# Optimization experiments

Measured on AMD Instinct MI355X. Metric: run time of the kernel, lower is better.

## Reference

```python
import jax, jax.numpy as jnp
from jax import lax
import numpy as np

SQRT2 = 1.4142135623730951
STYLE_DIM = 512
MOD_SCALE = 1.0 / np.sqrt(float(STYLE_DIM))          # EqualLinear modulation, lr_mul=1
MAP_SCALE = 0.01 / np.sqrt(float(STYLE_DIM))          # mapping EqualLinear, lr_mul=0.01
LR_MUL = 0.01


def _blur_kernel():
    k = np.array([1.0, 3.0, 3.0, 1.0], dtype=np.float32)
    k = k[None, :] * k[:, None]
    return jnp.asarray(k / k.sum())


def upfirdn2d(x, k, up=1, down=1, pad=(0, 0)):
    # torch upfirdn2d inserts (up-1) zeros AFTER each sample -> extra trailing pad of up-1
    C = x.shape[1]
    kern = jnp.tile(k[None, None], (C, 1, 1, 1))  # depthwise [C,1,kh,kw] (kernel symmetric, no flip needed)
    p = (pad[0], pad[1] + up - 1)
    return lax.conv_general_dilated(x, kern, (down, down), [p, p], lhs_dilation=(up, up),
                                    dimension_numbers=('NCHW', 'OIHW', 'NCHW'), feature_group_count=C)


def fused_lrelu(x, b):
    return jax.nn.leaky_relu(x + b.reshape(1, -1, 1, 1), 0.2) * SQRT2


def grouped_conv(x, w, pad, up):
    # x: [B,I,H,W], w: [B,O,I,k,k] per-sample weights -> grouped conv with B groups
    B, O, I, kh, kw = w.shape
    xg = x.reshape(1, B * I, x.shape[2], x.shape[3])
    if up:
        # torch conv_transpose2d(stride=2, padding=0) == dilated conv with spatially flipped kernel
        wf = jnp.flip(w, (-2, -1)).reshape(B * O, I, kh, kw)
        out = lax.conv_general_dilated(xg, wf, (1, 1), [(kh - 1, kh - 1), (kw - 1, kw - 1)],
                                       lhs_dilation=(2, 2),
                                       dimension_numbers=('NCHW', 'OIHW', 'NCHW'), feature_group_count=B)
    else:
        out = lax.conv_general_dilated(xg, w.reshape(B * O, I, kh, kw), (1, 1), [(pad, pad), (pad, pad)],
                                       dimension_numbers=('NCHW', 'OIHW', 'NCHW'), feature_group_count=B)
    return out.reshape(B, O, out.shape[2], out.shape[3])


def mod_conv(x, weight, style, mod_w, mod_b, demodulate, up, blur_k):
    # weight: [O,I,k,k]; style: [B,512]
    s = style @ (mod_w * MOD_SCALE).T + mod_b                       # [B,I]
    scale = 1.0 / np.sqrt(float(weight.shape[1] * weight.shape[2] * weight.shape[3]))
    w = scale * weight[None] * s[:, None, :, None, None]            # [B,O,I,k,k]
    if demodulate:
        d = lax.rsqrt(jnp.sum(w * w, axis=(2, 3, 4)) + 1e-8)
        w = w * d[:, :, None, None, None]
    out = grouped_conv(x, w, weight.shape[-1] // 2, up)
    if up:
        out = upfirdn2d(out, blur_k * 4.0, pad=(1, 1))              # Blur pad from p=len(k)-2-(3-1)=0
    return out


def _forward(z, mlp_w, mlp_b, const_input, conv_w, conv_mod_w, conv_mod_b, conv_bias,
             noise_strength, rgb_w, rgb_mod_w, rgb_mod_b, rgb_bias):
    B = z.shape[0]
    blur_k = _blur_kernel()
    w_lat = z * lax.rsqrt(jnp.mean(z * z, axis=1, keepdims=True) + 1e-8)
    for i in range(mlp_w.shape[0]):
        w_lat = jax.nn.leaky_relu(w_lat @ (mlp_w[i] * MAP_SCALE).T + mlp_b[i] * LR_MUL, 0.2) * SQRT2
    nkey = jax.random.key(7)

    def noise(l, shape):
        return jax.random.normal(jax.random.fold_in(nkey, l), (shape[0], 1, shape[2], shape[3]), dtype=jnp.float32)

    def styled(x, l, up):
        y = mod_conv(x, conv_w[l], w_lat, conv_mod_w[l], conv_mod_b[l], True, up, blur_k)
        y = y + noise_strength[l] * noise(l, y.shape)
        return fused_lrelu(y, conv_bias[l])

    def to_rgb(x, i):
        y = mod_conv(x, rgb_w[i], w_lat, rgb_mod_w[i], rgb_mod_b[i], False, False, blur_k)
        return y + rgb_bias[i].reshape(1, -1, 1, 1)

    out = jnp.tile(const_input, (B, 1, 1, 1))   # ConstantInput (shift=0 -> identity rolls)
    out = styled(out, 0, False)
    skip = to_rgb(out, 0)
    l = 1
    for blk in range(3):  # resolutions 8, 16, 32
        out = styled(out, l, True); l += 1
        out = styled(out, l, False); l += 1
        # Upsample(skip): kernel*factor^2, pad=(2,1), up=2
        skip = to_rgb(out, blk + 1) + upfirdn2d(skip, blur_k * 4.0, up=2, pad=(2, 1))
    return skip  # [B,3,32,32]


def setup_inputs() -> dict:
    key = jax.random.key(0)
    ks = jax.random.split(key, 8)
    B, S, C = 8, 512, 512
    return {
        'z': jax.random.normal(ks[0], (B, S), jnp.float32),
        'mlp_w': jax.random.normal(ks[1], (8, S, S), jnp.float32),
        'mlp_b': jnp.zeros((8, S), jnp.float32),
        'const_input': jax.random.normal(ks[2], (1, C, 4, 4), jnp.float32),
        'conv_w': jax.random.normal(ks[3], (7, C, C, 3, 3), jnp.float32),
        'conv_mod_w': jax.random.normal(ks[4], (7, C, S), jnp.float32),
        'conv_mod_b': jnp.ones((7, C), jnp.float32),
        'conv_bias': jnp.zeros((7, C), jnp.float32),
        'noise_strength': jax.random.normal(ks[5], (7,), jnp.float32) * 0.1,
        'rgb_w': jax.random.normal(ks[6], (4, 3, C, 1, 1), jnp.float32),
        'rgb_mod_w': jax.random.normal(ks[7], (4, C, S), jnp.float32),
        'rgb_mod_b': jnp.ones((4, C), jnp.float32),
        'rgb_bias': jnp.zeros((4, 3), jnp.float32),
    }


def reference(z, mlp_w, mlp_b, const_input, conv_w, conv_mod_w, conv_mod_b, conv_bias,
              noise_strength, rgb_w, rgb_mod_w, rgb_mod_b, rgb_bias):
    return _forward(z, mlp_w, mlp_b, const_input, conv_w, conv_mod_w, conv_mod_b, conv_bias,
                    noise_strength, rgb_w, rgb_mod_w, rgb_mod_b, rgb_bias)
```

## Files before the change

### kernel.cpp

```cpp
#include <hip/hip_runtime.h>


#define SQRT2F      1.41421356f
#define MAP_SCALE   4.41941738e-04f
#define MOD_SCALE   4.41941738e-02f
#define CONV_SCALE  1.47313913e-02f
#define RGB_SCALE   4.41941738e-02f

typedef __attribute__((ext_vector_type(8))) short bf16x8;
typedef __attribute__((ext_vector_type(16))) float f32x16;

__device__ __forceinline__ float bf2f(ushort u) {
    return __uint_as_float(((unsigned)u) << 16);
}
__device__ __forceinline__ ushort f2bf(float f) {
    unsigned u = __float_as_uint(f);
    unsigned r = (u + 0x7FFFu + ((u >> 16) & 1u)) >> 16;
    return (ushort)r;
}
__device__ __forceinline__ void store4bf(ushort* p, float a, float b, float c, float d) {
    union { ushort u[4]; uint2 v; } x;
    x.u[0] = f2bf(a); x.u[1] = f2bf(b); x.u[2] = f2bf(c); x.u[3] = f2bf(d);
    *(uint2*)p = x.v;
}

typedef __attribute__((address_space(1))) const unsigned int GAS;
typedef __attribute__((address_space(3))) unsigned int LAS;
__device__ __forceinline__ void gload_lds16(const ushort* g, ushort* l) {
    __builtin_amdgcn_global_load_lds((GAS*)g, (LAS*)l, 16, 0, 0);
}


__device__ __forceinline__ unsigned rotl32(unsigned x, int r) {
    return (x << r) | (x >> (32 - r));
}

__device__ void threefry2x32(unsigned k0, unsigned k1, unsigned x0, unsigned x1,
                             unsigned& o0, unsigned& o1) {
    unsigned k2 = k0 ^ k1 ^ 0x1BD11BDAu;
    x0 += k0; x1 += k1;
    x0 += x1; x1 = rotl32(x1,13); x1 ^= x0;
    x0 += x1; x1 = rotl32(x1,15); x1 ^= x0;
    x0 += x1; x1 = rotl32(x1,26); x1 ^= x0;
    x0 += x1; x1 = rotl32(x1, 6); x1 ^= x0;
    x0 += k1; x1 += k2 + 1u;
    x0 += x1; x1 = rotl32(x1,17); x1 ^= x0;
    x0 += x1; x1 = rotl32(x1,29); x1 ^= x0;
    x0 += x1; x1 = rotl32(x1,16); x1 ^= x0;
    x0 += x1; x1 = rotl32(x1,24); x1 ^= x0;
    x0 += k2; x1 += k0 + 2u;
    x0 += x1; x1 = rotl32(x1,13); x1 ^= x0;
    x0 += x1; x1 = rotl32(x1,15); x1 ^= x0;
    x0 += x1; x1 = rotl32(x1,26); x1 ^= x0;
    x0 += x1; x1 = rotl32(x1, 6); x1 ^= x0;
    x0 += k0; x1 += k1 + 3u;
    x0 += x1; x1 = rotl32(x1,17); x1 ^= x0;
    x0 += x1; x1 = rotl32(x1,29); x1 ^= x0;
    x0 += x1; x1 = rotl32(x1,16); x1 ^= x0;
    x0 += x1; x1 = rotl32(x1,24); x1 ^= x0;
    x0 += k1; x1 += k2 + 4u;
    x0 += x1; x1 = rotl32(x1,13); x1 ^= x0;
    x0 += x1; x1 = rotl32(x1,15); x1 ^= x0;
    x0 += x1; x1 = rotl32(x1,26); x1 ^= x0;
    x0 += x1; x1 = rotl32(x1, 6); x1 ^= x0;
    x0 += k2; x1 += k0 + 5u;
    o0 = x0; o1 = x1;
}

__device__ float bits_to_normal(unsigned bits) {
    unsigned m = (bits >> 9) | 0x3F800000u;
    float f = __uint_as_float(m) - 1.0f;
    const float lo = -0.99999994f;
    float u = f * 2.0f + lo;
    u = fmaxf(lo, u);
    float w = -log1pf(-u * u);
    float p;
    if (w < 5.0f) {
        w -= 2.5f;
        p = 2.81022636e-08f;
        p = fmaf(p, w, 3.43273939e-07f);
        p = fmaf(p, w, -3.5233877e-06f);
        p = fmaf(p, w, -4.39150654e-06f);
        p = fmaf(p, w, 0.00021858087f);
        p = fmaf(p, w, -0.00125372503f);
        p = fmaf(p, w, -0.00417768164f);
        p = fmaf(p, w, 0.246640727f);
        p = fmaf(p, w, 1.50140941f);
    } else {
        w = sqrtf(w) - 3.0f;
        p = -0.000200214257f;
        p = fmaf(p, w, 0.000100950558f);
        p = fmaf(p, w, 0.00134934322f);
        p = fmaf(p, w, -0.00367342844f);
        p = fmaf(p, w, 0.00573950773f);
        p = fmaf(p, w, -0.0076224613f);
        p = fmaf(p, w, 0.00943887047f);
        p = fmaf(p, w, 1.00167406f);
        p = fmaf(p, w, 2.83297682f);
    }
    return 1.41421354f * (p * u);
}

__global__ void noise_kernel(float* __restrict__ nbuf) {
    int g = blockIdx.x * 256 + threadIdx.x;
    if (g >= 21632) return;
    const int off[8] = {0, 128, 640, 1152, 3200, 5248, 13440, 21632};
    int l = 0;
    while (l < 6 && g >= off[l + 1]) l++;
    int i = g - off[l];
    unsigned k0, k1;
    threefry2x32(0u, 7u, 0u, (unsigned)l, k0, k1);
    unsigned b0, b1;
    threefry2x32(k0, k1, 0u, (unsigned)i, b0, b1);
    nbuf[g] = bits_to_normal(b0 ^ b1);
}


__global__ void pixelnorm_kernel(const float* __restrict__ z, float* __restrict__ out) {
    int b = blockIdx.x;
    int lane = threadIdx.x;
    float v[8];
    float s = 0.f;
    #pragma unroll
    for (int j = 0; j < 8; j++) {
        v[j] = z[b * 512 + lane + (j << 6)];
        s += v[j] * v[j];
    }
    #pragma unroll
    for (int off = 32; off > 0; off >>= 1) s += __shfl_xor(s, off, 64);
    float norm = rsqrtf(s * (1.f / 512.f) + 1e-8f);
    #pragma unroll
    for (int j = 0; j < 8; j++)
        out[b * 512 + lane + (j << 6)] = v[j] * norm;
}

__global__ void dot512_kernel(const float* __restrict__ win, const float* __restrict__ W,
                              const float* __restrict__ bias, float* __restrict__ out,
                              int total, float wscale, float bscale, int mode) {
    int gt = blockIdx.x * blockDim.x + threadIdx.x;
    int wv = gt >> 6;
    int lane = gt & 63;
    if (wv >= total) return;
    int l = wv >> 12;
    int r = wv & 4095;
    int b = r >> 9;
    int o = r & 511;
    const float* wrow = W + ((size_t)(l * 512 + o) << 9);
    const float* xrow = win + ((size_t)b << 9);
    float s = 0.f;
    #pragma unroll
    for (int j = 0; j < 8; j++) {
        int k = lane + (j << 6);
        s += wrow[k] * xrow[k];
    }
    #pragma unroll
    for (int off = 32; off > 0; off >>= 1) s += __shfl_xor(s, off, 64);
    if (lane == 0) {
        float v = s * wscale + bias[l * 512 + o] * bscale;
        if (mode) v = (v > 0.f ? v : 0.2f * v) * SQRT2F;
        out[wv] = v;
    }
}

__global__ __launch_bounds__(256) void wbconv_all(const float* __restrict__ cw,
                                                  ushort* __restrict__ wb7,
                                                  float* __restrict__ wsq7) {
    __shared__ float lg[288 * 65];
    const int bid = blockIdx.x;
    const int l = bid >> 7, rem = bid & 127, c = rem >> 3, og = rem & 7;
    const int o0 = og * 64;
    const int ibase = c * 32;
    const int tid = threadIdx.x;
    const int flip = (l == 1 || l == 3 || l == 5);

    #pragma unroll
    for (int r = 0; r < 18; r++) {
        int u = tid + 256 * r;
        int o = u / 72, w = u % 72;
        const float* src = cw + ((size_t)((l * 512 + o0 + o) * 512 + ibase)) * 9 + w * 4;
        float4 v = *(const float4*)src;
        lg[(w * 4 + 0) * 65 + o] = v.x;
        lg[(w * 4 + 1) * 65 + o] = v.y;
        lg[(w * 4 + 2) * 65 + o] = v.z;
        lg[(w * 4 + 3) * 65 + o] = v.w;
    }
    __syncthreads();

    #pragma unroll
    for (int r = 0; r < 8; r++) {
        int u = tid + 256 * r;
        int o = u >> 5, il = u & 31;
        float s = 0.f;
        #pragma unroll
        for (int t = 0; t < 9; t++) {
            float x = lg[(il * 9 + t) * 65 + o];
            s += x * x;
        }
        wsq7[((size_t)(l * 512 + o0 + o)) * 512 + ibase + il] = s;
    }

    ushort* wb = wb7 + (size_t)l * 2359296;
    #pragma unroll
    for (int r = 0; r < 9; r++) {
        int u = tid + 256 * r;
        int o = u & 63, tk = u >> 6;
        int t = tk >> 2, kv = tk & 3;
        int tsrc = flip ? (8 - t) : t;
        union { ushort us[8]; uint4 v; } pk;
        #pragma unroll
        for (int e = 0; e < 8; e++)
            pk.us[e] = f2bf(lg[((kv * 8 + e) * 9 + tsrc) * 65 + o]);
        *(uint4*)&wb[(size_t)(((c * 9 + t) * 4 + kv) * 512 + o0 + o) * 8] = pk.v;
    }
}

__global__ void demod_all(const float* __restrict__ wsq7, const float* __restrict__ sc,
                          float* __restrict__ dm) {
    int gt = blockIdx.x * blockDim.x + threadIdx.x;
    int wv = gt >> 6;
    int lane = gt & 63;
    if (wv >= 7 * 4096) return;
    int l = wv >> 12, b = (wv >> 9) & 7, o = wv & 511;
    const float* wr = wsq7 + (size_t)l * 262144 + ((size_t)o << 9);
    const float* sr = sc + l * 4096 + (b << 9);
    float s = 0.f;
    #pragma unroll
    for (int j = 0; j < 8; j++) {
        int k = lane + (j << 6);
        float sv = sr[k];
        s += wr[k] * sv * sv;
    }
    #pragma unroll
    for (int off = 32; off > 0; off >>= 1) s += __shfl_xor(s, off, 64);
    if (lane == 0) dm[wv] = rsqrtf(s * (1.f / 4608.f) + 1e-8f);
}

__global__ void prep0_kernel(const float* __restrict__ cinp, const float* __restrict__ s0,
                             ushort* __restrict__ X0p) {
    int gid = blockIdx.x * 256 + threadIdx.x;
    if (gid >= 8 * 36 * 64) return;
    int grp = gid & 63;
    int r = gid >> 6;
    int b = r / 36, rc = r % 36, row = rc / 6, col = rc % 6;
    int y = row - 1, x = col - 1;
    union { ushort u[8]; bf16x8 v; } pk;
    if (y >= 0 && y < 4 && x >= 0 && x < 4) {
        #pragma unroll
        for (int k = 0; k < 8; k++) {
            int ch = grp * 8 + k;
            pk.u[k] = f2bf(cinp[ch * 16 + y * 4 + x] * s0[b * 512 + ch]);
        }
    } else {
        #pragma unroll
        for (int k = 0; k < 8; k++) pk.u[k] = 0;
    }
    *(bf16x8*)&X0p[((size_t)grp * 288 + r) * 8] = pk.v;
}

template <int S, int NTILE, int WROWS, int KS, bool WUP>
__global__ __launch_bounds__(512, 1) void conv_dense6(
    const ushort* __restrict__ Xp, const ushort* __restrict__ wb,
    const float* __restrict__ dm, const float* __restrict__ nz,
    const float* __restrict__ nstr, const float* __restrict__ bias,
    const float* __restrict__ snext,
    ushort* __restrict__ T, ushort* __restrict__ XU, float* __restrict__ Pp) {
    constexpr int SP = S + 2, P2 = S * S, N = 8 * P2;
    constexpr int PXT = 8 * SP * SP;
    constexpr int JCOLS = NTILE / 128;
    constexpr int NPX = WROWS * SP;
    constexpr int ASZ = 9 * 4 * 64 * 8;
    constexpr int BSZ = NPX * 32;
    constexpr int PAIR = ASZ + BSZ;
    constexpr int NAU = 2304;
    constexpr int NAT = 5;
    constexpr int NBU = NPX * 4;
    constexpr int NBT = (NBU + 511) / 512;
    constexpr int ROWMAX = 8 * SP - 1;
    constexpr int CK = 16 / KS;
    constexpr int DB = (CK > 1) ? 2 : 1;
    constexpr int NAF = 4;
    constexpr int NBF = NBU / 512;
    constexpr int NMIN = NAF + NBF;
    constexpr int REDU = JCOLS * 16384;
    constexpr int LDSZ = (DB * PAIR > REDU) ? DB * PAIR : REDU;
    __shared__ __align__(16) ushort lds[LDSZ];

    const int tid = threadIdx.x, lane = tid & 63, nw = tid >> 6;
    const int sw = nw >> 2, nww = nw & 3;
    const int hf = lane >> 5, l31 = lane & 31;
    const int o0 = blockIdx.x * 64;
    const int n0 = blockIdx.y * NTILE;
    const int ks = blockIdx.z;
    const int R0 = (n0 / P2) * SP + (n0 % P2) / S;
    const int kvw = sw * 2 + hf;

    int pixbase[JCOLS], nj[JCOLS];
    #pragma unroll
    for (int j = 0; j < JCOLS; j++) {
        int n = n0 + nww * (NTILE / 4) + j * 32 + l31;
        nj[j] = n;
        int b = n / P2, r = n % P2;
        int y = r / S, x = r % S;
        pixbase[j] = (b * SP + y - R0) * SP + x;
    }
    f32x16 acc[JCOLS][2];
    #pragma unroll
    for (int j = 0; j < JCOLS; j++) { acc[j][0] = (f32x16)0.f; acc[j][1] = (f32x16)0.f; }

    int bgo[NBT];
    bool bgv[NBT];
    #pragma unroll
    for (int r = 0; r < NBT; r++) {
        int t = tid + 512 * r;
        bgv[r] = t < NBU;
        int tt = bgv[r] ? t : 0;
        int px = tt % NPX, kv = tt / NPX;
        int rr = px / SP, cc = px % SP;
        int Rc = R0 + rr; if (Rc > ROWMAX) Rc = ROWMAX;
        bgo[r] = (kv * PXT + Rc * SP + cc) * 8;
    }

    auto stage = [&](int cgi, int buf) {
        ushort* base = &lds[buf * PAIR];
        const ushort* asrc = wb + (size_t)cgi * 147456;
        #pragma unroll
        for (int r = 0; r < NAT; r++) {
            int u = tid + 512 * r;
            if (u < NAU) {
                int row = u >> 6;
                gload_lds16(asrc + ((size_t)(row * 512 + o0) + (u & 63)) * 8,
                            base + (r * 512 + nw * 64) * 8);
            }
        }
        const ushort* bsrc = Xp + (size_t)cgi * (PXT * 32);
        #pragma unroll
        for (int r = 0; r < NBT; r++)
            if (bgv[r])
                gload_lds16(bsrc + bgo[r], base + ASZ + (r * 512 + nw * 64) * 8);
    };

    stage(ks * CK, 0);
    for (int c = 0; c < CK; c++) {
        const int cur = c & 1;
        if (c + 1 < CK) {
            stage(ks * CK + c + 1, cur ^ 1);
            asm volatile("s_waitcnt vmcnt(%0)" :: "i"(NMIN) : "memory");
        } else {
            asm volatile("s_waitcnt vmcnt(0)" ::: "memory");
        }
        __builtin_amdgcn_s_barrier();
        __builtin_amdgcn_sched_barrier(0);
        const int bo = cur * PAIR;
        #pragma unroll
        for (int t = 0; t < 9; t++) {
            const int dpx = (t / 3) * SP + (t % 3);
            bf16x8 a0 = *(const bf16x8*)&lds[bo + ((t * 4 + kvw) * 64 + l31) * 8];
            bf16x8 a1 = *(const bf16x8*)&lds[bo + ((t * 4 + kvw) * 64 + 32 + l31) * 8];
            #pragma unroll
            for (int j = 0; j < JCOLS; j++) {
                bf16x8 bf = *(const bf16x8*)&lds[bo + ASZ + (kvw * NPX + pixbase[j] + dpx) * 8];
                acc[j][0] = __builtin_amdgcn_mfma_f32_32x32x16_bf16(a0, bf, acc[j][0], 0, 0, 0);
                acc[j][1] = __builtin_amdgcn_mfma_f32_32x32x16_bf16(a1, bf, acc[j][1], 0, 0, 0);
            }
        }
        __builtin_amdgcn_sched_barrier(0);
        __builtin_amdgcn_s_barrier();
    }

    #pragma unroll
    for (int j = 0; j < JCOLS; j++)
        #pragma unroll
        for (int sub = 0; sub < 2; sub++)
            #pragma unroll
            for (int rq = 0; rq < 4; rq++)
                if (sw == 1) {
                    int sidx = (j * 2 + sub) * 4 + rq;
                    float4 v = make_float4(acc[j][sub][rq * 4 + 0], acc[j][sub][rq * 4 + 1],
                                           acc[j][sub][rq * 4 + 2], acc[j][sub][rq * 4 + 3]);
                    *(float4*)&lds[sidx * 2048 + (nww * 64 + lane) * 8] = v;
                }
    __syncthreads();
    if (sw == 1) return;
    #pragma unroll
    for (int j = 0; j < JCOLS; j++)
        #pragma unroll
        for (int sub = 0; sub < 2; sub++)
            #pragma unroll
            for (int rq = 0; rq < 4; rq++) {
                int sidx = (j * 2 + sub) * 4 + rq;
                float4 p = *(const float4*)&lds[sidx * 2048 + (nww * 64 + lane) * 8];
                acc[j][sub][rq * 4 + 0] += p.x;
                acc[j][sub][rq * 4 + 1] += p.y;
                acc[j][sub][rq * 4 + 2] += p.z;
                acc[j][sub][rq * 4 + 3] += p.w;
            }

    if constexpr (KS > 1) {
        #pragma unroll
        for (int j = 0; j < JCOLS; j++) {
            float* pb = Pp + (((size_t)(ks * N + nj[j])) << 9) + o0;
            #pragma unroll
            for (int sub = 0; sub < 2; sub++) {
                #pragma unroll
                for (int rq = 0; rq < 4; rq++) {
                    float4 v = make_float4(acc[j][sub][rq * 4 + 0], acc[j][sub][rq * 4 + 1],
                                           acc[j][sub][rq * 4 + 2], acc[j][sub][rq * 4 + 3]);
                    *(float4*)&pb[sub * 32 + 4 * hf + 8 * rq] = v;
                }
            }
        }
        return;
    }
    float ns = nstr[0];
    #pragma unroll
    for (int j = 0; j < JCOLS; j++) {
        int n = nj[j], b = n / P2, r = n % P2;
        float nv = nz[b * P2 + r];
        int y = r / S, x = r % S;
        size_t tbase = (size_t)n << 9;
        int gpx = (b * SP + y + 1) * SP + x + 1;
        #pragma unroll
        for (int sub = 0; sub < 2; sub++) {
            #pragma unroll
            for (int rq = 0; rq < 4; rq++) {
                int o = o0 + sub * 32 + 4 * hf + 8 * rq;
                float4 d4 = *(const float4*)&dm[b * 512 + o];
                float4 b4 = *(const float4*)&bias[o];
                float vv[4];
                #pragma unroll
                for (int ri = 0; ri < 4; ri++) {
                    float v = acc[j][sub][rq * 4 + ri] * (&d4.x)[ri] * CONV_SCALE
                              + ns * nv + (&b4.x)[ri];
                    vv[ri] = (v > 0.f ? v : 0.2f * v) * SQRT2F;
                }
                store4bf(T + tbase + o, vv[0], vv[1], vv[2], vv[3]);
                if (WUP) {
                    float4 s4 = *(const float4*)&snext[b * 512 + o];
                    store4bf(XU + ((size_t)(o >> 3) * PXT + gpx) * 8 + (o & 7),
                             vv[0] * s4.x, vv[1] * s4.y, vv[2] * s4.z, vv[3] * s4.w);
                }
            }
        }
    }
}

template <int S, int KS, bool WUP>
__global__ void combine_dense(const float* __restrict__ Pp, const float* __restrict__ dm,
                              const float* __restrict__ nz, const float* __restrict__ nstr,
                              const float* __restrict__ bias, const float* __restrict__ snext,
                              ushort* __restrict__ T, ushort* __restrict__ XU) {
    constexpr int P2 = S * S, N = 8 * P2, SP = S + 2;
    constexpr int PXT = 8 * SP * SP;
    int gid = blockIdx.x * 256 + threadIdx.x;
    int n = gid >> 7, og = (gid & 127) << 2;
    float4 sm = make_float4(0.f, 0.f, 0.f, 0.f);
    #pragma unroll
    for (int k = 0; k < KS; k++) {
        float4 p = *(const float4*)&Pp[(((size_t)(k * N + n)) << 9) + og];
        sm.x += p.x; sm.y += p.y; sm.z += p.z; sm.w += p.w;
    }
    int b = n / P2, r = n % P2;
    float nsv = nstr[0] * nz[b * P2 + r];
    float4 d4 = *(const float4*)&dm[b * 512 + og];
    float4 b4 = *(const float4*)&bias[og];
    float vv[4];
    const float* sp = &sm.x;
    #pragma unroll
    for (int i = 0; i < 4; i++) {
        float v = sp[i] * (&d4.x)[i] * CONV_SCALE + nsv + (&b4.x)[i];
        vv[i] = (v > 0.f ? v : 0.2f * v) * SQRT2F;
    }
    store4bf(&T[((size_t)n << 9) + og], vv[0], vv[1], vv[2], vv[3]);
    if (WUP) {
        int y = r / S, x = r % S;
        int gpx = (b * SP + y + 1) * SP + x + 1;
        float4 s4 = *(const float4*)&snext[b * 512 + og];
        store4bf(&XU[((size_t)(og >> 3) * PXT + gpx) * 8 + (og & 7)],
                 vv[0] * s4.x, vv[1] * s4.y, vv[2] * s4.z, vv[3] * s4.w);
    }
}

template <int HIN, int NTILE, int WRW>
__global__ __launch_bounds__(256, 2) void conv_up5(
    const ushort* __restrict__ Xp, const ushort* __restrict__ wb,
    const float* __restrict__ dm, ushort* __restrict__ U) {
    constexpr int SPI = HIN + 2, SOUT = 2 * HIN + 1, SPO = SOUT + 2;
    constexpr int PXT = 8 * SPI * SPI;
    constexpr int PXTO = 8 * SPO * SPO;
    constexpr int JCOLS = NTILE / 128;
    constexpr int NPX = WRW * SPI;
    constexpr int ASZ = 4 * 4 * 64 * 8;
    constexpr int BSZ = NPX * 32;
    constexpr int PAIR = ASZ + BSZ;
    constexpr int NBU = NPX * 4;
    constexpr int NBT = (NBU + 255) / 256;
    constexpr int ROWMAX = 8 * SPI - 1;
    constexpr int MINB = (NBU > 192) ? ((NBU - 192 + 255) / 256) : 0;
    constexpr int NMIN = 4 + MINB;
    __shared__ __align__(16) ushort lds[2 * PAIR];

    const int py = blockIdx.z >> 1, pxp = blockIdx.z & 1;
    const int GY = py ? HIN : HIN + 1, GX = pxp ? HIN : HIN + 1;
    const int GG = GY * GX, NCLS = 8 * GG;
    const int NTY = py ? 1 : 2, NTX = pxp ? 1 : 2, NT = NTY * NTX;
    const int n0 = blockIdx.y * NTILE;
    if (n0 >= NCLS) return;

    int taplist[4], toffs[4];
    {
        int k = 0;
        #pragma unroll
        for (int a2 = 0; a2 < 2; a2++) {
            if (a2 >= NTY) break;
            int dy = py ? 1 : a2 * 2;
            #pragma unroll
            for (int c2 = 0; c2 < 2; c2++) {
                if (c2 >= NTX) break;
                int dx = pxp ? 1 : c2 * 2;
                taplist[k] = dy * 3 + dx;
                toffs[k] = ((dy + py) >> 1) * SPI + ((dx + pxp) >> 1);
                k++;
            }
        }
        for (; k < 4; k++) { taplist[k] = 0; toffs[k] = 0; }
    }

    const int tid = threadIdx.x, lane = tid & 63, nw = tid >> 6;
    const int hf = lane >> 5, l31 = lane & 31;
    const int o0 = blockIdx.x * 64;
    const int R0 = (n0 / GG) * SPI + (n0 % GG) / GX;

    int pixbase[JCOLS], bj[JCOLS], gyj[JCOLS], gxj[JCOLS];
    bool validj[JCOLS];
    #pragma unroll
    for (int j = 0; j < JCOLS; j++) {
        int n = n0 + nw * (NTILE / 4) + j * 32 + l31;
        validj[j] = n < NCLS;
        int nc = validj[j] ? n : (NCLS - 1);
        int b = nc / GG, rem = nc % GG;
        int gy = rem / GX, gx = rem % GX;
        bj[j] = b; gyj[j] = gy; gxj[j] = gx;
        pixbase[j] = (b * SPI + gy - R0) * SPI + gx;
    }
    f32x16 acc[JCOLS][2];
    #pragma unroll
    for (int j = 0; j < JCOLS; j++) { acc[j][0] = (f32x16)0.f; acc[j][1] = (f32x16)0.f; }

    int bgo[NBT];
    bool bgv[NBT];
    #pragma unroll
    for (int r = 0; r < NBT; r++) {
        int t = tid + 256 * r;
        bgv[r] = t < NBU;
        int tt = bgv[r] ? t : 0;
        int px = tt % NPX, kv = tt / NPX;
        int rr = px / SPI, cc = px % SPI;
        int Rc = R0 + rr; if (Rc > ROWMAX) Rc = ROWMAX;
        bgo[r] = (kv * PXT + Rc * SPI + cc) * 8;
    }
    const int aoff = (nw * 512 + o0 + lane) * 8;
    int atap[4];
    #pragma unroll
    for (int r = 0; r < 4; r++) atap[r] = taplist[r] * 16384;

    auto stage = [&](int cgi, int buf) {
        ushort* dstA = &lds[buf * PAIR + nw * 512];
        ushort* dstB = &lds[buf * PAIR + ASZ + nw * 512];
        const ushort* asrc = wb + (size_t)cgi * 147456 + aoff;
        #pragma unroll
        for (int r = 0; r < 4; r++)
            gload_lds16(asrc + atap[r], dstA + r * 2048);
        const ushort* bsrc = Xp + (size_t)cgi * (PXT * 32);
        #pragma unroll
        for (int r = 0; r < NBT; r++)
            if (bgv[r])
                gload_lds16(bsrc + bgo[r], dstB + r * 2048);
    };

    stage(0, 0);
    for (int c = 0; c < 16; c++) {
        const int cur = c & 1;
        if (c + 1 < 16) {
            stage(c + 1, cur ^ 1);
            asm volatile("s_waitcnt vmcnt(%0)" :: "i"(NMIN) : "memory");
        } else {
            asm volatile("s_waitcnt vmcnt(0)" ::: "memory");
        }
        __builtin_amdgcn_s_barrier();
        __builtin_amdgcn_sched_barrier(0);
        const int bo = cur * PAIR;
        for (int tt = 0; tt < NT; ++tt) {
            const int dpx = toffs[tt];
            #pragma unroll
            for (int s = 0; s < 2; s++) {
                const int kv = s * 2 + hf;
                bf16x8 a0 = *(const bf16x8*)&lds[bo + ((tt * 4 + kv) * 64 + l31) * 8];
                bf16x8 a1 = *(const bf16x8*)&lds[bo + ((tt * 4 + kv) * 64 + 32 + l31) * 8];
                #pragma unroll
                for (int j = 0; j < JCOLS; j++) {
                    bf16x8 bf = *(const bf16x8*)&lds[bo + ASZ + (kv * NPX + pixbase[j] + dpx) * 8];
                    acc[j][0] = __builtin_amdgcn_mfma_f32_32x32x16_bf16(a0, bf, acc[j][0], 0, 0, 0);
                    acc[j][1] = __builtin_amdgcn_mfma_f32_32x32x16_bf16(a1, bf, acc[j][1], 0, 0, 0);
                }
            }
        }
        __builtin_amdgcn_sched_barrier(0);
        __builtin_amdgcn_s_barrier();
    }
    #pragma unroll
    for (int j = 0; j < JCOLS; j++) {
        if (!validj[j]) continue;
        int b = bj[j];
        int y = 2 * gyj[j] + py, x = 2 * gxj[j] + pxp;
        int gpx = (b * SPO + y + 1) * SPO + x + 1;
        #pragma unroll
        for (int sub = 0; sub < 2; sub++) {
            #pragma unroll
            for (int rq = 0; rq < 4; rq++) {
                int o = o0 + sub * 32 + 4 * hf + 8 * rq;
                float4 d4 = *(const float4*)&dm[b * 512 + o];
                float vv[4];
                #pragma unroll
                for (int ri = 0; ri < 4; ri++)
                    vv[ri] = acc[j][sub][rq * 4 + ri] * (&d4.x)[ri] * CONV_SCALE;
                store4bf(U + ((size_t)(o >> 3) * PXTO + gpx) * 8 + (o & 7),
                         vv[0], vv[1], vv[2], vv[3]);
            }
        }
    }
}

template <int SIN>
__global__ void blur_px(const ushort* __restrict__ U, const float* __restrict__ nz,
                        const float* __restrict__ nstr, const float* __restrict__ bias,
                        const float* __restrict__ snext, ushort* __restrict__ X) {
    constexpr int O = SIN - 1, SPI = SIN + 2, SPO = O + 2;
    constexpr int PXTU = 8 * SPI * SPI;
    constexpr int PXTO = 8 * SPO * SPO;
    int gid = blockIdx.x * 256 + threadIdx.x;
    if (gid >= 8 * O * O * 64) return;
    int grp = gid & 63;
    int pxl = gid >> 6;
    int b = pxl / (O * O), r = pxl % (O * O), u = r / O, vcol = r % O;
    const float k1[4] = {0.25f, 0.75f, 0.75f, 0.25f};
    float acc[8];
    #pragma unroll
    for (int k = 0; k < 8; k++) acc[k] = 0.f;
    const ushort* Ug = U + (size_t)grp * PXTU * 8;
    #pragma unroll
    for (int a = 0; a < 4; a++) {
        int row = b * SPI + u + a;
        #pragma unroll
        for (int c = 0; c < 4; c++) {
            float w = k1[a] * k1[c];
            bf16x8 v = *(const bf16x8*)&Ug[(size_t)(row * SPI + vcol + c) * 8];
            #pragma unroll
            for (int k = 0; k < 8; k++) acc[k] += w * bf2f((ushort)v[k]);
        }
    }
    float nsv = nstr[0] * nz[b * O * O + r];
    float4 b0 = *(const float4*)&bias[grp * 8];
    float4 b1 = *(const float4*)&bias[grp * 8 + 4];
    float4 s0 = *(const float4*)&snext[b * 512 + grp * 8];
    float4 s1 = *(const float4*)&snext[b * 512 + grp * 8 + 4];
    union { ushort us[8]; bf16x8 v; } pk;
    #pragma unroll
    for (int k = 0; k < 8; k++) {
        float bk = (k < 4) ? (&b0.x)[k] : (&b1.x)[k - 4];
        float sk = (k < 4) ? (&s0.x)[k] : (&s1.x)[k - 4];
        float v = acc[k] + nsv + bk;
        v = (v > 0.f ? v : 0.2f * v) * SQRT2F;
        pk.us[k] = f2bf(v * sk);
    }
    *(bf16x8*)&X[((size_t)grp * PXTO + (b * SPO + u + 1) * SPO + vcol + 1) * 8] = pk.v;
}

template <int H>
__global__ void skipup_kernel(const float* __restrict__ skip, float* __restrict__ out) {
    constexpr int O = 2 * H;
    int idx = blockIdx.x * 256 + threadIdx.x;
    if (idx >= 8 * 3 * O * O) return;
    int px = idx % (O * O);
    int bc = idx / (O * O);
    int u = px / O, v = px % O;
    const float k1[4] = {0.25f, 0.75f, 0.75f, 0.25f};
    const float* src = skip + (size_t)bc * (H * H);
    float acc = 0.f;
    #pragma unroll
    for (int ty = 0; ty < 4; ty++) {
        int r = u + ty - 2;
        if (r < 0 || (r & 1) || (r >> 1) >= H) continue;
        float rsum = 0.f;
        #pragma unroll
        for (int tx = 0; tx < 4; tx++) {
            int cc = v + tx - 2;
            if (cc < 0 || (cc & 1) || (cc >> 1) >= H) continue;
            rsum += k1[tx] * src[(r >> 1) * H + (cc >> 1)];
        }
        acc += k1[ty] * rsum;
    }
    out[(size_t)bc * (O * O) + px] = acc;
}

__global__ void torgb_px(const ushort* __restrict__ T, int P2,
                         const float* __restrict__ rgbw, const float* __restrict__ srgb,
                         const float* __restrict__ rbias, const float* __restrict__ skipup,
                         float* __restrict__ dst) {
    int b = blockIdx.x;
    int px = blockIdx.y * 4 + (threadIdx.x >> 6);
    int lane = threadIdx.x & 63;
    int c8 = lane * 8;
    bf16x8 v = *(const bf16x8*)&T[(((size_t)b * P2 + px) << 9) + c8];
    float4 sa = *(const float4*)&srgb[b * 512 + c8];
    float4 sb = *(const float4*)&srgb[b * 512 + c8 + 4];
    float xs[8];
    #pragma unroll
    for (int k = 0; k < 8; k++) {
        float sk = (k < 4) ? (&sa.x)[k] : (&sb.x)[k - 4];
        xs[k] = bf2f((ushort)v[k]) * sk;
    }
    float sums[3];
    #pragma unroll
    for (int c = 0; c < 3; c++) {
        float4 w0 = *(const float4*)&rgbw[c * 512 + c8];
        float4 w1 = *(const float4*)&rgbw[c * 512 + c8 + 4];
        float s = 0.f;
        #pragma unroll
        for (int k = 0; k < 8; k++) {
            float wk = (k < 4) ? (&w0.x)[k] : (&w1.x)[k - 4];
            s += xs[k] * wk;
        }
        #pragma unroll
        for (int off = 32; off > 0; off >>= 1) s += __shfl_xor(s, off, 64);
        sums[c] = s;
    }
    if (lane == 0) {
        #pragma unroll
        for (int c = 0; c < 3; c++) {
            float o = sums[c] * RGB_SCALE + rbias[c];
            if (skipup) o += skipup[((size_t)b * 3 + c) * P2 + px];
            dst[((size_t)b * 3 + c) * P2 + px] = o;
        }
    }
}


extern "C" void kernel_launch(void* const* d_in, const int* in_sizes, int n_in,
                              void* d_out, int out_size, void* d_ws, size_t ws_size,
                              hipStream_t stream) {
    const float* z      = (const float*)d_in[0];
    const float* mlp_w  = (const float*)d_in[1];
    const float* mlp_b  = (const float*)d_in[2];
    const float* cinp   = (const float*)d_in[3];
    const float* conv_w = (const float*)d_in[4];
    const float* cmw    = (const float*)d_in[5];
    const float* cmb    = (const float*)d_in[6];
    const float* cbias  = (const float*)d_in[7];
    const float* nstr   = (const float*)d_in[8];
    const float* rgbw   = (const float*)d_in[9];
    const float* rmw    = (const float*)d_in[10];
    const float* rmb    = (const float*)d_in[11];
    const float* rbias  = (const float*)d_in[12];
    float* out = (float*)d_out;
    float* ws = (float*)d_ws;

    float* wlatA = ws;
    float* wlatB = ws + 4096;
    float* sconv = ws + 8192;
    float* srgb  = ws + 36864;
    float* dem   = ws + 53248;
    float* noise = ws + 81920;
    float* skipA = ws + 103552;
    float* skipB = ws + 128128;
    float* skipU = ws + 152704;
    float* wsq7  = ws + 177280;
    ushort* wbuf7 = (ushort*)(ws + 2012288);
    float* Ppart = ws + 10269824;
    ushort* A1 = (ushort*)(ws + 12366976);
    ushort* A2 = (ushort*)(ws + 14875776);
    ushort* A3 = (ushort*)(ws + 17243264);

    ushort* X0p = A1;
    ushort* T0  = A2;
    ushort* XU1 = A3;
    ushort* U1  = A1;
    ushort* X2  = A2;
    ushort* T2  = A3;
    ushort* XU3 = A1;
    ushort* U3  = A2;
    ushort* X4  = A1;
    ushort* T4  = A2;
    ushort* XU5 = A3;
    ushort* U5  = A1;
    ushort* X6  = A2;
    ushort* T6  = A3;

    const size_t LWB = 2359296;

    wbconv_all<<<896, 256, 0, stream>>>(conv_w, wbuf7, wsq7);
    noise_kernel<<<85, 256, 0, stream>>>(noise);

    pixelnorm_kernel<<<8, 64, 0, stream>>>(z, wlatA);
    float* a = wlatA;
    float* bb = wlatB;
    for (int i = 0; i < 8; i++) {
        dot512_kernel<<<1024, 256, 0, stream>>>(a, mlp_w + (size_t)i * 262144,
                                                mlp_b + i * 512, bb, 4096,
                                                MAP_SCALE, 0.01f, 1);
        float* t = a; a = bb; bb = t;
    }
    dot512_kernel<<<7168, 256, 0, stream>>>(a, cmw, cmb, sconv, 7 * 4096, MOD_SCALE, 1.0f, 0);
    dot512_kernel<<<4096, 256, 0, stream>>>(a, rmw, rmb, srgb, 4 * 4096, MOD_SCALE, 1.0f, 0);
    demod_all<<<7168, 256, 0, stream>>>(wsq7, sconv, dem);
    prep0_kernel<<<72, 256, 0, stream>>>(cinp, sconv, X0p);

    conv_dense6<4, 128, 48, 16, false><<<dim3(8, 1, 16), 512, 0, stream>>>(
        X0p, wbuf7, nullptr, nullptr, nullptr, nullptr, nullptr,
        nullptr, nullptr, Ppart);
    hipMemsetAsync(XU1, 0, (size_t)8 * 36 * 512 * 2, stream);
    combine_dense<4, 16, true><<<64, 256, 0, stream>>>(
        Ppart, dem, noise, nstr, cbias, sconv + 4096, T0, XU1);
    torgb_px<<<dim3(8, 4), 256, 0, stream>>>(T0, 16, rgbw, srgb, rbias, nullptr, skipA);

    hipMemsetAsync(U1, 0, (size_t)8 * 121 * 512 * 2, stream);
    conv_up5<4, 128, 48><<<dim3(8, 2, 4), 256, 0, stream>>>(XU1, wbuf7 + LWB, dem + 4096, U1);
    hipMemsetAsync(X2, 0, (size_t)8 * 100 * 512 * 2, stream);
    blur_px<9><<<128, 256, 0, stream>>>(U1, noise + 128, nstr + 1, cbias + 512,
                                        sconv + 2 * 4096, X2);

    conv_dense6<8, 128, 20, 8, false><<<dim3(8, 4, 8), 512, 0, stream>>>(
        X2, wbuf7 + 2 * LWB, nullptr, nullptr, nullptr, nullptr, nullptr,
        nullptr, nullptr, Ppart);
    hipMemsetAsync(XU3, 0, (size_t)8 * 100 * 512 * 2, stream);
    combine_dense<8, 8, true><<<256, 256, 0, stream>>>(
        Ppart, dem + 2 * 4096, noise + 640, nstr + 2, cbias + 2 * 512,
        sconv + 3 * 4096, T2, XU3);
    skipup_kernel<4><<<6, 256, 0, stream>>>(skipA, skipU);
    torgb_px<<<dim3(8, 16), 256, 0, stream>>>(T2, 64, rgbw + 1536, srgb + 4096,
                                              rbias + 3, skipU, skipB);

    hipMemsetAsync(U3, 0, (size_t)8 * 361 * 512 * 2, stream);
    conv_up5<8, 128, 22><<<dim3(8, 6, 4), 256, 0, stream>>>(XU3, wbuf7 + 3 * LWB,
                                                            dem + 3 * 4096, U3);
    hipMemsetAsync(X4, 0, (size_t)8 * 324 * 512 * 2, stream);
    blur_px<17><<<512, 256, 0, stream>>>(U3, noise + 1152, nstr + 3, cbias + 3 * 512,
                                         sconv + 4 * 4096, X4);

    conv_dense6<16, 128, 10, 2, false><<<dim3(8, 16, 2), 512, 0, stream>>>(
        X4, wbuf7 + 4 * LWB, nullptr, nullptr, nullptr, nullptr, nullptr,
        nullptr, nullptr, Ppart);
    hipMemsetAsync(XU5, 0, (size_t)8 * 324 * 512 * 2, stream);
    combine_dense<16, 2, true><<<1024, 256, 0, stream>>>(
        Ppart, dem + 4 * 4096, noise + 3200, nstr + 4, cbias + 4 * 512,
        sconv + 5 * 4096, T4, XU5);
    skipup_kernel<8><<<24, 256, 0, stream>>>(skipB, skipU);
    torgb_px<<<dim3(8, 64), 256, 0, stream>>>(T4, 256, rgbw + 2 * 1536, srgb + 2 * 4096,
                                              rbias + 6, skipU, skipA);

    hipMemsetAsync(U5, 0, (size_t)8 * 1225 * 512 * 2, stream);
    conv_up5<16, 256, 20><<<dim3(8, 10, 4), 256, 0, stream>>>(XU5, wbuf7 + 5 * LWB,
                                                              dem + 5 * 4096, U5);
    hipMemsetAsync(X6, 0, (size_t)8 * 1156 * 512 * 2, stream);
    blur_px<33><<<2048, 256, 0, stream>>>(U5, noise + 5248, nstr + 5, cbias + 5 * 512,
                                          sconv + 6 * 4096, X6);

    conv_dense6<32, 256, 10, 1, false><<<dim3(8, 32, 1), 512, 0, stream>>>(
        X6, wbuf7 + 6 * LWB, dem + 6 * 4096, noise + 13440, nstr + 6, cbias + 6 * 512,
        nullptr, T6, nullptr, nullptr);
    skipup_kernel<16><<<96, 256, 0, stream>>>(skipA, skipU);
    torgb_px<<<dim3(8, 256), 256, 0, stream>>>(T6, 1024, rgbw + 3 * 1536, srgb + 3 * 4096,
                                               rbias + 9, skipU, out);
}
```

Baseline: 404.0 us.

## Split conv taps across wave groups in new conv_dense7 and swap grid axes

Adds conv_dense7, which partitions the 9 conv taps between two wave halves and the pixel tile between two more, then reduces the partial accumulators through LDS in a two-level tree. It is used for the 16x16 and 32x32 dense convolutions. All conv launches also swap grid x/y so that consecutive blocks walk pixel tiles rather than output-channel tiles, which changes L2 reuse of weights versus activations. The tap split cuts per-wave MFMA serial work but adds extra LDS reduction passes and barriers.

```diff
diff --git a/kernel.cpp b/kernel.cpp
--- a/kernel.cpp
+++ b/kernel.cpp
@@ -288,8 +288,8 @@
     const int tid = threadIdx.x, lane = tid & 63, nw = tid >> 6;
     const int sw = nw >> 2, nww = nw & 3;
     const int hf = lane >> 5, l31 = lane & 31;
-    const int o0 = blockIdx.x * 64;
-    const int n0 = blockIdx.y * NTILE;
+    const int o0 = blockIdx.y * 64;
+    const int n0 = blockIdx.x * NTILE;
     const int ks = blockIdx.z;
     const int R0 = (n0 / P2) * SP + (n0 % P2) / S;
     const int kvw = sw * 2 + hf;
@@ -394,6 +394,206 @@
                 acc[j][sub][rq * 4 + 2] += p.z;
                 acc[j][sub][rq * 4 + 3] += p.w;
             }
+
+    if constexpr (KS > 1) {
+        #pragma unroll
+        for (int j = 0; j < JCOLS; j++) {
+            float* pb = Pp + (((size_t)(ks * N + nj[j])) << 9) + o0;
+            #pragma unroll
+            for (int sub = 0; sub < 2; sub++) {
+                #pragma unroll
+                for (int rq = 0; rq < 4; rq++) {
+                    float4 v = make_float4(acc[j][sub][rq * 4 + 0], acc[j][sub][rq * 4 + 1],
+                                           acc[j][sub][rq * 4 + 2], acc[j][sub][rq * 4 + 3]);
+                    *(float4*)&pb[sub * 32 + 4 * hf + 8 * rq] = v;
+                }
+            }
+        }
+        return;
+    }
+    float ns = nstr[0];
+    #pragma unroll
+    for (int j = 0; j < JCOLS; j++) {
+        int n = nj[j], b = n / P2, r = n % P2;
+        float nv = nz[b * P2 + r];
+        int y = r / S, x = r % S;
+        size_t tbase = (size_t)n << 9;
+        int gpx = (b * SP + y + 1) * SP + x + 1;
+        #pragma unroll
+        for (int sub = 0; sub < 2; sub++) {
+            #pragma unroll
+            for (int rq = 0; rq < 4; rq++) {
+                int o = o0 + sub * 32 + 4 * hf + 8 * rq;
+                float4 d4 = *(const float4*)&dm[b * 512 + o];
+                float4 b4 = *(const float4*)&bias[o];
+                float vv[4];
+                #pragma unroll
+                for (int ri = 0; ri < 4; ri++) {
+                    float v = acc[j][sub][rq * 4 + ri] * (&d4.x)[ri] * CONV_SCALE
+                              + ns * nv + (&b4.x)[ri];
+                    vv[ri] = (v > 0.f ? v : 0.2f * v) * SQRT2F;
+                }
+                store4bf(T + tbase + o, vv[0], vv[1], vv[2], vv[3]);
+                if (WUP) {
+                    float4 s4 = *(const float4*)&snext[b * 512 + o];
+                    store4bf(XU + ((size_t)(o >> 3) * PXT + gpx) * 8 + (o & 7),
+                             vv[0] * s4.x, vv[1] * s4.y, vv[2] * s4.z, vv[3] * s4.w);
+                }
+            }
+        }
+    }
+}
+
+template <int S, int NTILE, int WROWS, int KS, bool WUP>
+__global__ __launch_bounds__(512, 1) void conv_dense7(
+    const ushort* __restrict__ Xp, const ushort* __restrict__ wb,
+    const float* __restrict__ dm, const float* __restrict__ nz,
+    const float* __restrict__ nstr, const float* __restrict__ bias,
+    const float* __restrict__ snext,
+    ushort* __restrict__ T, ushort* __restrict__ XU, float* __restrict__ Pp) {
+    constexpr int SP = S + 2, P2 = S * S, N = 8 * P2;
+    constexpr int PXT = 8 * SP * SP;
+    constexpr int JCOLS = NTILE / 64;
+    constexpr int NPX = WROWS * SP;
+    constexpr int ASZ = 9 * 4 * 64 * 8;
+    constexpr int BSZ = NPX * 32;
+    constexpr int PAIR = ASZ + BSZ;
+    constexpr int NAU = 2304;
+    constexpr int NAT = 5;
+    constexpr int NBU = NPX * 4;
+    constexpr int NBT = (NBU + 511) / 512;
+    constexpr int ROWMAX = 8 * SP - 1;
+    constexpr int CK = 16 / KS;
+    constexpr int DB = (CK > 1) ? 2 : 1;
+    constexpr int NAF = 4;
+    constexpr int NBF = NBU / 512;
+    constexpr int NMIN = NAF + NBF;
+    constexpr int SLOTUS = JCOLS * 4096;
+    constexpr int REDU = 4 * SLOTUS;
+    constexpr int LDSZ = (DB * PAIR > REDU) ? DB * PAIR : REDU;
+    __shared__ __align__(16) ushort lds[LDSZ];
+
+    const int tid = threadIdx.x, lane = tid & 63, nw = tid >> 6;
+    const int sw = nw >> 2, th = (nw >> 1) & 1, nh = nw & 1;
+    const int hf = lane >> 5, l31 = lane & 31;
+    const int o0 = blockIdx.y * 64;
+    const int n0 = blockIdx.x * NTILE;
+    const int ks = blockIdx.z;
+    const int R0 = (n0 / P2) * SP + (n0 % P2) / S;
+    const int kvw = sw * 2 + hf;
+
+    int pixbase[JCOLS], nj[JCOLS];
+    #pragma unroll
+    for (int j = 0; j < JCOLS; j++) {
+        int n = n0 + nh * (NTILE / 2) + j * 32 + l31;
+        nj[j] = n;
+        int b = n / P2, r = n % P2;
+        int y = r / S, x = r % S;
+        pixbase[j] = (b * SP + y - R0) * SP + x;
+    }
+    f32x16 acc[JCOLS][2];
+    #pragma unroll
+    for (int j = 0; j < JCOLS; j++) { acc[j][0] = (f32x16)0.f; acc[j][1] = (f32x16)0.f; }
+
+    int bgo[NBT];
+    bool bgv[NBT];
+    #pragma unroll
+    for (int r = 0; r < NBT; r++) {
+        int t = tid + 512 * r;
+        bgv[r] = t < NBU;
+        int tt = bgv[r] ? t : 0;
+        int px = tt % NPX, kv = tt / NPX;
+        int rr = px / SP, cc = px % SP;
+        int Rc = R0 + rr; if (Rc > ROWMAX) Rc = ROWMAX;
+        bgo[r] = (kv * PXT + Rc * SP + cc) * 8;
+    }
+
+    auto stage = [&](int cgi, int buf) {
+        ushort* base = &lds[buf * PAIR];
+        const ushort* asrc = wb + (size_t)cgi * 147456;
+        #pragma unroll
+        for (int r = 0; r < NAT; r++) {
+            int u = tid + 512 * r;
+            if (u < NAU) {
+                int row = u >> 6;
+                gload_lds16(asrc + ((size_t)(row * 512 + o0) + (u & 63)) * 8,
+                            base + (r * 512 + nw * 64) * 8);
+            }
+        }
+        const ushort* bsrc = Xp + (size_t)cgi * (PXT * 32);
+        #pragma unroll
+        for (int r = 0; r < NBT; r++)
+            if (bgv[r])
+                gload_lds16(bsrc + bgo[r], base + ASZ + (r * 512 + nw * 64) * 8);
+    };
+
+    stage(ks * CK, 0);
+    for (int c = 0; c < CK; c++) {
+        const int cur = c & 1;
+        if (c + 1 < CK) {
+            stage(ks * CK + c + 1, cur ^ 1);
+            asm volatile("s_waitcnt vmcnt(%0)" :: "i"(NMIN) : "memory");
+        } else {
+            asm volatile("s_waitcnt vmcnt(0)" ::: "memory");
+        }
+        __builtin_amdgcn_s_barrier();
+        __builtin_amdgcn_sched_barrier(0);
+        const int bo = cur * PAIR;
+        #pragma unroll
+        for (int tl = 0; tl < 5; tl++) {
+            const int t = th * 5 + tl;
+            if (t < 9) {
+                const int dpx = (t / 3) * SP + (t % 3);
+                bf16x8 a0 = *(const bf16x8*)&lds[bo + ((t * 4 + kvw) * 64 + l31) * 8];
+                bf16x8 a1 = *(const bf16x8*)&lds[bo + ((t * 4 + kvw) * 64 + 32 + l31) * 8];
+                #pragma unroll
+                for (int j = 0; j < JCOLS; j++) {
+                    bf16x8 bf = *(const bf16x8*)&lds[bo + ASZ + (kvw * NPX + pixbase[j] + dpx) * 8];
+                    acc[j][0] = __builtin_amdgcn_mfma_f32_32x32x16_bf16(a0, bf, acc[j][0], 0, 0, 0);
+                    acc[j][1] = __builtin_amdgcn_mfma_f32_32x32x16_bf16(a1, bf, acc[j][1], 0, 0, 0);
+                }
+            }
+        }
+        __builtin_amdgcn_sched_barrier(0);
+        __builtin_amdgcn_s_barrier();
+    }
+
+    auto spillacc = [&](int slot) {
+        #pragma unroll
+        for (int j = 0; j < JCOLS; j++)
+            #pragma unroll
+            for (int sub = 0; sub < 2; sub++)
+                #pragma unroll
+                for (int rq = 0; rq < 4; rq++) {
+                    int sidx = (j * 2 + sub) * 4 + rq;
+                    float4 v = make_float4(acc[j][sub][rq * 4 + 0], acc[j][sub][rq * 4 + 1],
+                                           acc[j][sub][rq * 4 + 2], acc[j][sub][rq * 4 + 3]);
+                    *(float4*)&lds[slot * SLOTUS + sidx * 512 + lane * 8] = v;
+                }
+    };
+    auto addacc = [&](int slot) {
+        #pragma unroll
+        for (int j = 0; j < JCOLS; j++)
+            #pragma unroll
+            for (int sub = 0; sub < 2; sub++)
+                #pragma unroll
+                for (int rq = 0; rq < 4; rq++) {
+                    int sidx = (j * 2 + sub) * 4 + rq;
+                    float4 p = *(const float4*)&lds[slot * SLOTUS + sidx * 512 + lane * 8];
+                    acc[j][sub][rq * 4 + 0] += p.x;
+                    acc[j][sub][rq * 4 + 1] += p.y;
+                    acc[j][sub][rq * 4 + 2] += p.z;
+                    acc[j][sub][rq * 4 + 3] += p.w;
+                }
+    };
+    if (sw == 1) spillacc(th * 2 + nh);
+    __syncthreads();
+    if (sw == 0) addacc(th * 2 + nh);
+    __syncthreads();
+    if (sw == 0 && th == 1) spillacc(nh);
+    __syncthreads();
+    if (!(sw == 0 && th == 0)) return;
+    addacc(nh);
 
     if constexpr (KS > 1) {
         #pragma unroll
@@ -503,7 +703,7 @@
     const int GY = py ? HIN : HIN + 1, GX = pxp ? HIN : HIN + 1;
     const int GG = GY * GX, NCLS = 8 * GG;
     const int NTY = py ? 1 : 2, NTX = pxp ? 1 : 2, NT = NTY * NTX;
-    const int n0 = blockIdx.y * NTILE;
+    const int n0 = blockIdx.x * NTILE;
     if (n0 >= NCLS) return;
 
     int taplist[4], toffs[4];
@@ -527,7 +727,7 @@
 
     const int tid = threadIdx.x, lane = tid & 63, nw = tid >> 6;
     const int hf = lane >> 5, l31 = lane & 31;
-    const int o0 = blockIdx.x * 64;
+    const int o0 = blockIdx.y * 64;
     const int R0 = (n0 / GG) * SPI + (n0 % GG) / GX;
 
     int pixbase[JCOLS], bj[JCOLS], gyj[JCOLS], gxj[JCOLS];
@@ -814,7 +1014,7 @@
     demod_all<<<7168, 256, 0, stream>>>(wsq7, sconv, dem);
     prep0_kernel<<<72, 256, 0, stream>>>(cinp, sconv, X0p);
 
-    conv_dense6<4, 128, 48, 16, false><<<dim3(8, 1, 16), 512, 0, stream>>>(
+    conv_dense6<4, 128, 48, 16, false><<<dim3(1, 8, 16), 512, 0, stream>>>(
         X0p, wbuf7, nullptr, nullptr, nullptr, nullptr, nullptr,
         nullptr, nullptr, Ppart);
     hipMemsetAsync(XU1, 0, (size_t)8 * 36 * 512 * 2, stream);
@@ -823,12 +1023,12 @@
     torgb_px<<<dim3(8, 4), 256, 0, stream>>>(T0, 16, rgbw, srgb, rbias, nullptr, skipA);
 
     hipMemsetAsync(U1, 0, (size_t)8 * 121 * 512 * 2, stream);
-    conv_up5<4, 128, 48><<<dim3(8, 2, 4), 256, 0, stream>>>(XU1, wbuf7 + LWB, dem + 4096, U1);
+    conv_up5<4, 128, 48><<<dim3(2, 8, 4), 256, 0, stream>>>(XU1, wbuf7 + LWB, dem + 4096, U1);
     hipMemsetAsync(X2, 0, (size_t)8 * 100 * 512 * 2, stream);
     blur_px<9><<<128, 256, 0, stream>>>(U1, noise + 128, nstr + 1, cbias + 512,
                                         sconv + 2 * 4096, X2);
 
-    conv_dense6<8, 128, 20, 8, false><<<dim3(8, 4, 8), 512, 0, stream>>>(
+    conv_dense6<8, 128, 20, 8, false><<<dim3(4, 8, 8), 512, 0, stream>>>(
         X2, wbuf7 + 2 * LWB, nullptr, nullptr, nullptr, nullptr, nullptr,
         nullptr, nullptr, Ppart);
     hipMemsetAsync(XU3, 0, (size_t)8 * 100 * 512 * 2, stream);
@@ -840,13 +1040,13 @@
                                               rbias + 3, skipU, skipB);
 
     hipMemsetAsync(U3, 0, (size_t)8 * 361 * 512 * 2, stream);
-    conv_up5<8, 128, 22><<<dim3(8, 6, 4), 256, 0, stream>>>(XU3, wbuf7 + 3 * LWB,
+    conv_up5<8, 128, 22><<<dim3(6, 8, 4), 256, 0, stream>>>(XU3, wbuf7 + 3 * LWB,
                                                             dem + 3 * 4096, U3);
     hipMemsetAsync(X4, 0, (size_t)8 * 324 * 512 * 2, stream);
     blur_px<17><<<512, 256, 0, stream>>>(U3, noise + 1152, nstr + 3, cbias + 3 * 512,
                                          sconv + 4 * 4096, X4);
 
-    conv_dense6<16, 128, 10, 2, false><<<dim3(8, 16, 2), 512, 0, stream>>>(
+    conv_dense7<16, 128, 10, 2, false><<<dim3(16, 8, 2), 512, 0, stream>>>(
         X4, wbuf7 + 4 * LWB, nullptr, nullptr, nullptr, nullptr, nullptr,
         nullptr, nullptr, Ppart);
     hipMemsetAsync(XU5, 0, (size_t)8 * 324 * 512 * 2, stream);
@@ -858,13 +1058,13 @@
                                               rbias + 6, skipU, skipA);
 
     hipMemsetAsync(U5, 0, (size_t)8 * 1225 * 512 * 2, stream);
-    conv_up5<16, 256, 20><<<dim3(8, 10, 4), 256, 0, stream>>>(XU5, wbuf7 + 5 * LWB,
+    conv_up5<16, 256, 20><<<dim3(10, 8, 4), 256, 0, stream>>>(XU5, wbuf7 + 5 * LWB,
                                                               dem + 5 * 4096, U5);
     hipMemsetAsync(X6, 0, (size_t)8 * 1156 * 512 * 2, stream);
     blur_px<33><<<2048, 256, 0, stream>>>(U5, noise + 5248, nstr + 5, cbias + 5 * 512,
                                           sconv + 6 * 4096, X6);
 
-    conv_dense6<32, 256, 10, 1, false><<<dim3(8, 32, 1), 512, 0, stream>>>(
+    conv_dense7<32, 256, 10, 1, false><<<dim3(32, 8, 1), 512, 0, stream>>>(
         X6, wbuf7 + 6 * LWB, dem + 6 * 4096, noise + 13440, nstr + 6, cbias + 6 * 512,
         nullptr, T6, nullptr, nullptr);
     skipup_kernel<16><<<96, 256, 0, stream>>>(skipA, skipU);
```

New measurement: 408.6 us. Within noise of the previous version (+1.1%).
